# Kernel tuning notes

Measured on AMD Instinct MI355X. Metric: run time of the kernel, lower is better.

The kernel has to match this reference:

```python
import jax, jax.numpy as jnp
import numpy as np

B, IN, OUT = 8192, 4096, 2048  # OUT must equal 32*64 per betta/gamma sizes


def setup_inputs() -> dict:
    key = jax.random.key(0)
    kx, kw = jax.random.split(key, 2)
    X = jax.random.normal(kx, (B, IN), dtype=jnp.float32)
    # xavier-uniform-like init for W
    limit = float(np.sqrt(6.0 / (IN + OUT)))
    W = jax.random.uniform(kw, (IN, OUT), minval=-limit, maxval=limit, dtype=jnp.float32)
    absmean = jnp.abs(W).mean(axis=0)
    alpha = jnp.abs(W).mean()          # scalar, >= 0
    betta = absmean[:32]               # (32,), >= 0
    gamma = absmean[32:96]             # (64,), >= 0
    return {"X": X, "W": W, "alpha": alpha, "betta": betta, "gamma": gamma}


def reference(X, W, alpha, betta, gamma):
    # module applies relu_ to alpha/betta/gamma data before the functional call
    alpha = jax.nn.relu(alpha)
    betta = jax.nn.relu(betta)
    gamma = jax.nn.relu(gamma)
    X_bin = jnp.sign(X)                # (B, IN)
    W_bin = jnp.sign(W)                # (IN, OUT)
    # scale[i*64+j] = alpha * betta[i] * gamma[j] -> (OUT,)
    scale = (alpha * jnp.outer(betta, gamma)).reshape(-1)
    return (X_bin @ W_bin) * scale     # (B, OUT)
```

## Files before the change

kernel.cpp:

```cpp
#include <hip/hip_runtime.h>


#define M_DIM 8192
#define K_DIM 4096
#define N_DIM 2048
#define NT    (K_DIM / 256)
#define TILE_BYTES 32768
#define PANEL_BYTES (NT * TILE_BYTES)

typedef int i32x4 __attribute__((ext_vector_type(4)));
typedef int i32x8 __attribute__((ext_vector_type(8)));
typedef float f32x16 __attribute__((ext_vector_type(16)));

__device__ __forceinline__ unsigned int nib4(float x) {
  unsigned int s = (__float_as_uint(x) >> 28) & 0x8u;
  return x == 0.0f ? 0u : (0x2u | s);
}

__device__ __forceinline__ unsigned int pack8(const float* f) {
  unsigned int p = 0;
#pragma unroll
  for (int j = 0; j < 8; ++j) p |= nib4(f[j]) << (4 * j);
  return p;
}

__device__ __forceinline__ void gload_lds16(const void* g, void* lds) {
  __builtin_amdgcn_global_load_lds(
      (const __attribute__((address_space(1))) unsigned int*)g,
      (__attribute__((address_space(3))) unsigned int*)lds, 16, 0, 0);
}

__device__ __forceinline__ i32x8 pad8(i32x4 v) {
  i32x8 r;
  r[0] = v[0]; r[1] = v[1]; r[2] = v[2]; r[3] = v[3];
  r[4] = 0; r[5] = 0; r[6] = 0; r[7] = 0;
  return r;
}

__global__ __launch_bounds__(256) void binXW_kernel(
    const float* __restrict__ X, const float* __restrict__ W,
    unsigned char* __restrict__ Xq, unsigned char* __restrict__ Wq) {
  __shared__ float tile[32][257];
  const int t = threadIdx.x;
  const int bid = blockIdx.x;

  if (bid < 512) {
    const int p = bid >> 4;
    const int kt = bid & 15;
    const float* Xrow = X + (size_t)(p * 256 + t) * K_DIM + kt * 256;
    unsigned char* dst = Xq + (size_t)p * PANEL_BYTES + kt * TILE_BYTES;
#pragma unroll
    for (int s = 0; s < 8; ++s) {
      float f[32];
#pragma unroll
      for (int i = 0; i < 8; ++i)
        *(float4*)&f[i * 4] = *(const float4*)&Xrow[s * 32 + i * 4];
      uint4 gq;
      gq.x = pack8(f + 0);  gq.y = pack8(f + 8);
      gq.z = pack8(f + 16); gq.w = pack8(f + 24);
      *(uint4*)&dst[(s * 256 + t) * 16] = gq;
    }
  } else {
    const int idx = bid - 512;
    const int q = idx >> 4;
    const int kt = idx & 15;
    unsigned char* dst = Wq + (size_t)q * PANEL_BYTES + kt * TILE_BYTES;
    for (int s = 0; s < 8; ++s) {
#pragma unroll
      for (int it = 0; it < 8; ++it) {
        int row = it * 4 + (t >> 6);
        int col4 = (t & 63) * 4;
        *(float4*)&tile[row][col4] =
            *(const float4*)&W[(size_t)(kt * 256 + s * 32 + row) * N_DIM + q * 256 + col4];
      }
      __syncthreads();
      float f[32];
#pragma unroll
      for (int k = 0; k < 32; ++k) f[k] = tile[k][t];
      uint4 gq;
      gq.x = pack8(f + 0);  gq.y = pack8(f + 8);
      gq.z = pack8(f + 16); gq.w = pack8(f + 24);
      *(uint4*)&dst[(s * 256 + t) * 16] = gq;
      __syncthreads();
    }
  }
}

__device__ __forceinline__ void stage_tile(const unsigned char* __restrict__ src,
                                           unsigned char* lds, int t) {
#pragma unroll
  for (int p = 0; p < 4; ++p) {
    int c = p * 512 + t;
    gload_lds16(src + c * 16, lds + c * 16);
  }
}

__global__ __launch_bounds__(512, 2) void gemm_fp4_kernel(
    const unsigned char* __restrict__ Aq,
    const unsigned char* __restrict__ Bq,
    const float* __restrict__ alpha,
    const float* __restrict__ betta,
    const float* __restrict__ gamma,
    float* __restrict__ C) {
  __shared__ __align__(16) unsigned char smem[131072];

  const int t = threadIdx.x;
  const int lane = t & 63;
  const int l31 = lane & 31;
  const int lhi = lane >> 5;
  const int w = t >> 6;
  const int wr = w >> 2;
  const int wc = w & 3;

  const int bid = blockIdx.x;
  const int bn = bid & 7;
  const int bm = bid >> 3;
  const int row0 = bm * 256;
  const int col0 = bn * 256;

  const unsigned char* Abase = Aq + (size_t)bm * PANEL_BYTES;
  const unsigned char* Bbase = Bq + (size_t)bn * PANEL_BYTES;

  f32x16 acc[4][2];
#pragma unroll
  for (int fm = 0; fm < 4; ++fm)
#pragma unroll
    for (int fn = 0; fn < 2; ++fn)
#pragma unroll
      for (int r = 0; r < 16; ++r) acc[fm][fn][r] = 0.f;

  stage_tile(Abase, &smem[0], t);
  stage_tile(Bbase, &smem[32768], t);
  asm volatile("s_waitcnt vmcnt(0)" ::: "memory");
  __builtin_amdgcn_s_barrier();

  for (int kt = 0; kt < NT; ++kt) {
    const int cur = kt & 1;
    const unsigned char* pA = &smem[cur * 65536];
    const unsigned char* pB = pA + 32768;

#pragma unroll
    for (int kk = 0; kk < 4; ++kk) {
      const int g = kk * 2 + lhi;
      i32x4 a4[4], b4[2];
#pragma unroll
      for (int fm = 0; fm < 4; ++fm)
        a4[fm] = *(const i32x4*)&pA[(g * 256 + wr * 128 + fm * 32 + l31) * 16];
#pragma unroll
      for (int fn = 0; fn < 2; ++fn)
        b4[fn] = *(const i32x4*)&pB[(g * 256 + wc * 64 + fn * 32 + l31) * 16];

      if (kk == 0 && kt + 1 < NT)
        stage_tile(Abase + (kt + 1) * TILE_BYTES, &smem[(cur ^ 1) * 65536], t);
      if (kk == 1 && kt + 1 < NT)
        stage_tile(Bbase + (kt + 1) * TILE_BYTES, &smem[(cur ^ 1) * 65536 + 32768], t);

      __builtin_amdgcn_s_barrier();
      asm volatile("s_waitcnt lgkmcnt(0)" ::: "memory");
      __builtin_amdgcn_sched_barrier(0);
      __builtin_amdgcn_s_setprio(1);
#pragma unroll
      for (int fm = 0; fm < 4; ++fm) {
        i32x8 av = pad8(a4[fm]);
#pragma unroll
        for (int fn = 0; fn < 2; ++fn)
          acc[fm][fn] = __builtin_amdgcn_mfma_scale_f32_32x32x64_f8f6f4(
              av, pad8(b4[fn]), acc[fm][fn], 4, 4,
              0, 0x7F7F7F7F, 0, 0x7F7F7F7F);
      }
      __builtin_amdgcn_s_setprio(0);
    }
    asm volatile("s_waitcnt vmcnt(0)" ::: "memory");
    __builtin_amdgcn_s_barrier();
  }

  const float ra = fmaxf(alpha[0], 0.0f);
#pragma unroll
  for (int fn = 0; fn < 2; ++fn) {
    const int col = col0 + wc * 64 + fn * 32 + l31;
    const float sc = ra * fmaxf(betta[col >> 6], 0.0f) * fmaxf(gamma[col & 63], 0.0f);
#pragma unroll
    for (int fm = 0; fm < 4; ++fm) {
      const int rbase = row0 + wr * 128 + fm * 32 + 4 * lhi;
#pragma unroll
      for (int r = 0; r < 16; ++r) {
        const int row = rbase + (r & 3) + 8 * (r >> 2);
        C[(size_t)row * N_DIM + col] = acc[fm][fn][r] * sc;
      }
    }
  }
}

extern "C" void kernel_launch(void* const* d_in, const int* in_sizes, int n_in,
                              void* d_out, int out_size, void* d_ws, size_t ws_size,
                              hipStream_t stream) {
  const float* X = (const float*)d_in[0];
  const float* W = (const float*)d_in[1];
  const float* alpha = (const float*)d_in[2];
  const float* betta = (const float*)d_in[3];
  const float* gamma = (const float*)d_in[4];
  float* out = (float*)d_out;

  unsigned char* Xq = (unsigned char*)d_ws;
  unsigned char* Wq = Xq + (size_t)(M_DIM / 256) * PANEL_BYTES;

  binXW_kernel<<<640, 256, 0, stream>>>(X, W, Xq, Wq);
  gemm_fp4_kernel<<<(M_DIM / 256) * (N_DIM / 256), 512, 0, stream>>>(
      Xq, Wq, alpha, betta, gamma, out);
}
```

Measured before the change: 81.28 us.

## Split binarization into separate X and W kernels with finer-grained blocks

Replaces the single combined binarization kernel (640 blocks, each looping over 8 sub-slices) with two kernels: binX launches 4096 blocks where each thread packs one 32-element chunk, and binW launches 1024 blocks each handling one 32x256 transpose tile. The goal is more parallelism and memory-level concurrency in the bandwidth-bound quantization pass. The W tile padding also changes from 257 to 260 floats per row. In exchange it adds an extra kernel launch, and the new X mapping has each warp's threads reading rows 16KB apart with scattered 16-byte stores.

Result: faster. 76.05 us (-6.4%).

```diff
diff --git a/kernel.cpp b/kernel.cpp
--- a/kernel.cpp
+++ b/kernel.cpp
@@ -37,53 +37,54 @@
   return r;
 }
 
-__global__ __launch_bounds__(256) void binXW_kernel(
-    const float* __restrict__ X, const float* __restrict__ W,
-    unsigned char* __restrict__ Xq, unsigned char* __restrict__ Wq) {
-  __shared__ float tile[32][257];
+__global__ __launch_bounds__(256) void binX_kernel(
+    const float* __restrict__ X, unsigned char* __restrict__ Xq) {
   const int t = threadIdx.x;
-  const int bid = blockIdx.x;
-
-  if (bid < 512) {
-    const int p = bid >> 4;
-    const int kt = bid & 15;
-    const float* Xrow = X + (size_t)(p * 256 + t) * K_DIM + kt * 256;
-    unsigned char* dst = Xq + (size_t)p * PANEL_BYTES + kt * TILE_BYTES;
-#pragma unroll
-    for (int s = 0; s < 8; ++s) {
-      float f[32];
-#pragma unroll
-      for (int i = 0; i < 8; ++i)
-        *(float4*)&f[i * 4] = *(const float4*)&Xrow[s * 32 + i * 4];
-      uint4 gq;
-      gq.x = pack8(f + 0);  gq.y = pack8(f + 8);
-      gq.z = pack8(f + 16); gq.w = pack8(f + 24);
-      *(uint4*)&dst[(s * 256 + t) * 16] = gq;
-    }
-  } else {
-    const int idx = bid - 512;
-    const int q = idx >> 4;
-    const int kt = idx & 15;
-    unsigned char* dst = Wq + (size_t)q * PANEL_BYTES + kt * TILE_BYTES;
-    for (int s = 0; s < 8; ++s) {
-#pragma unroll
-      for (int it = 0; it < 8; ++it) {
-        int row = it * 4 + (t >> 6);
-        int col4 = (t & 63) * 4;
-        *(float4*)&tile[row][col4] =
-            *(const float4*)&W[(size_t)(kt * 256 + s * 32 + row) * N_DIM + q * 256 + col4];
-      }
-      __syncthreads();
-      float f[32];
-#pragma unroll
-      for (int k = 0; k < 32; ++k) f[k] = tile[k][t];
-      uint4 gq;
-      gq.x = pack8(f + 0);  gq.y = pack8(f + 8);
-      gq.z = pack8(f + 16); gq.w = pack8(f + 24);
-      *(uint4*)&dst[(s * 256 + t) * 16] = gq;
-      __syncthreads();
-    }
-  }
+  const int s = t >> 5;
+  const int r = t & 31;
+  const int rg = blockIdx.x >> 4;
+  const int kt = blockIdx.x & 15;
+  const int row = rg * 32 + r;
+  const int panel = row >> 8;
+
+  const float* src = X + (size_t)row * K_DIM + kt * 256 + s * 32;
+  float f[32];
+#pragma unroll
+  for (int i = 0; i < 8; ++i)
+    *(float4*)&f[i * 4] = *(const float4*)&src[i * 4];
+  uint4 gq;
+  gq.x = pack8(f + 0);  gq.y = pack8(f + 8);
+  gq.z = pack8(f + 16); gq.w = pack8(f + 24);
+  unsigned char* dst = Xq + (size_t)panel * PANEL_BYTES + kt * TILE_BYTES +
+                       ((size_t)s * 256 + (row & 255)) * 16;
+  *(uint4*)dst = gq;
+}
+
+__global__ __launch_bounds__(256) void binW_kernel(
+    const float* __restrict__ W, unsigned char* __restrict__ Wq) {
+  __shared__ float tile[32][260];
+  const int t = threadIdx.x;
+  const int q = blockIdx.x >> 7;
+  const int kt = (blockIdx.x >> 3) & 15;
+  const int s = blockIdx.x & 7;
+
+#pragma unroll
+  for (int i = 0; i < 8; ++i) {
+    int row = i * 4 + (t >> 6);
+    int col4 = (t & 63) * 4;
+    *(float4*)&tile[row][col4] =
+        *(const float4*)&W[(size_t)(kt * 256 + s * 32 + row) * N_DIM + q * 256 + col4];
+  }
+  __syncthreads();
+  float f[32];
+#pragma unroll
+  for (int k = 0; k < 32; ++k) f[k] = tile[k][t];
+  uint4 gq;
+  gq.x = pack8(f + 0);  gq.y = pack8(f + 8);
+  gq.z = pack8(f + 16); gq.w = pack8(f + 24);
+  unsigned char* dst = Wq + (size_t)q * PANEL_BYTES + kt * TILE_BYTES +
+                       ((size_t)s * 256 + t) * 16;
+  *(uint4*)dst = gq;
 }
 
 __device__ __forceinline__ void stage_tile(const unsigned char* __restrict__ src,
@@ -204,7 +205,8 @@
   unsigned char* Xq = (unsigned char*)d_ws;
   unsigned char* Wq = Xq + (size_t)(M_DIM / 256) * PANEL_BYTES;
 
-  binXW_kernel<<<640, 256, 0, stream>>>(X, W, Xq, Wq);
+  binW_kernel<<<1024, 256, 0, stream>>>(W, Wq);
+  binX_kernel<<<4096, 256, 0, stream>>>(X, Xq);
   gemm_fp4_kernel<<<(M_DIM / 256) * (N_DIM / 256), 512, 0, stream>>>(
       Xq, Wq, alpha, betta, gamma, out);
 }
```
